# Performance work log

Hardware: AMD Instinct MI355X
Metric: run time of the kernel (lower is better)

The kernel has to match this reference:

```python
import jax, jax.numpy as jnp
import numpy as np

N0, N1, N2 = 16384, 4096, 1024   # node counts at the 3 hierarchy levels
DEG = 16                          # avg degree -> E = N*DEG per level
OUT_CH = 4
GTD = 2048                        # global_token_dim


def _gcn(x, ei, w, b):
    # GCNConv: out = D^{-1/2} (A + I) D^{-1/2} (x @ W) + b
    n = x.shape[0]
    h = x @ w
    loop = jnp.arange(n, dtype=ei.dtype)
    src = jnp.concatenate([ei[0], loop])
    dst = jnp.concatenate([ei[1], loop])
    deg = jax.ops.segment_sum(jnp.ones(src.shape[0], h.dtype), dst, num_segments=n)
    dinv = jax.lax.rsqrt(jnp.maximum(deg, 1.0))   # deg >= 1 thanks to self loops
    coef = (dinv[src] * dinv[dst])[:, None]
    return jax.ops.segment_sum(h[src] * coef, dst, num_segments=n) + b


def _knn_interp(x, pos_src, pos_dst, k):
    # inverse-squared-distance weighted interpolation over k nearest sources
    d2 = (jnp.sum(pos_dst * pos_dst, -1, keepdims=True)
          + jnp.sum(pos_src * pos_src, -1)[None, :]
          - 2.0 * (pos_dst @ pos_src.T))          # (M, N) squared distances
    negd, idx = jax.lax.top_k(-d2, k)
    w = 1.0 / jnp.maximum(-negd, 1e-16)           # (M, k)
    return jnp.einsum('mk,mkc->mc', w, x[idx]) / jnp.sum(w, -1, keepdims=True)


def _bnorm(h, gamma, beta):
    # BatchNorm1d in training mode (batch statistics over nodes)
    mu = jnp.mean(h, 0)
    var = jnp.mean((h - mu) ** 2, 0)
    return (h - mu) * jax.lax.rsqrt(var + 1e-5) * gamma + beta


def _forward(fl, idx0, idx1, ei0, ei1, ei2):
    (x, pos,
     s1w0, s1b0, s1w1, s1b1, s1w2, s1b2,
     s2w0, s2b0, s2w1, s2b1, s2w2, s2b2,
     bw0, bb0, bw1, bb1, bw2, bb2,
     gw0, gb0, gw1, gb1, gw2, gb2, gg0, gbe0, gg1, gbe1,
     f2w0, f2b0, f2w1, f2b1, f2w2, f2b2,
     f1w0, f1b0, f1w1, f1b1, f1w2, f1b2,
     mw0, mb0, mw1, mb1) = fl
    relu = jax.nn.relu
    # SA1 (skip_pos_encoding=True): convs on full graph, then subsample by idx0
    h = relu(_gcn(x, ei0, s1w0, s1b0))
    h = relu(_gcn(h, ei0, s1w1, s1b1))
    h = relu(_gcn(h, ei0, s1w2, s1b2))
    x1, pos1 = h[idx0], pos[idx0]                 # (N1, 64)
    # SA2: concat pos, convs on level-1 graph, subsample by idx1
    h = jnp.concatenate([x1, pos1], 1)
    h = relu(_gcn(h, ei1, s2w0, s2b0))
    h = relu(_gcn(h, ei1, s2w1, s2b1))
    h = relu(_gcn(h, ei1, s2w2, s2b2))
    x2, pos2 = h[idx1], pos1[idx1]                # (N2, 128)
    # bottleneck (no subsample)
    h = jnp.concatenate([x2, pos2], 1)
    h = relu(_gcn(h, ei2, bw0, bb0))
    h = relu(_gcn(h, ei2, bw1, bb1))
    xb = relu(_gcn(h, ei2, bw2, bb2))             # (N2, 256)
    # GlobalSA: MLP(+BN) -> global max pool -> k=1 interp (broadcast, B=1) -> concat skip
    g = jnp.concatenate([x2, pos2], 1)
    g = relu(_bnorm(g @ gw0 + gb0, gg0, gbe0))
    g = relu(_bnorm(g @ gw1 + gb1, gg1, gbe1))
    g = g @ gw2 + gb2                             # (N2, GTD)
    gmax = jnp.max(g, 0, keepdims=True)
    h = jnp.concatenate([jnp.broadcast_to(gmax, (x2.shape[0], gmax.shape[1])), xb], 1)
    # FP2: knn-interpolate level2 -> level1, concat skip, convs on level-1 graph
    h = _knn_interp(h, pos2, pos1, 3)
    h = jnp.concatenate([h, x1], 1)               # (N1, GTD+256+64)
    h = relu(_gcn(h, ei1, f2w0, f2b0))
    h = relu(_gcn(h, ei1, f2w1, f2b1))
    h = relu(_gcn(h, ei1, f2w2, f2b2))
    # FP1: knn-interpolate level1 -> level0, concat raw features, convs on full graph
    h = _knn_interp(h, pos1, pos, 3)
    h = jnp.concatenate([h, x], 1)                # (N0, 518)
    h = relu(_gcn(h, ei0, f1w0, f1b0))
    h = relu(_gcn(h, ei0, f1w1, f1b1))
    h = relu(_gcn(h, ei0, f1w2, f1b2))            # (N0, 128)
    # final MLP (norm=None)
    return relu(h @ mw0 + mb0) @ mw1 + mb1        # (N0, OUT_CH)


def setup_inputs() -> dict:
    keys = iter(jax.random.split(jax.random.key(0), 64))
    def lin(i, o):
        return (jax.random.normal(next(keys), (i, o), jnp.float32) / np.float32(np.sqrt(i)),
                jnp.zeros((o,), jnp.float32))
    d = {}
    d['x'] = jax.random.normal(next(keys), (N0, 6), jnp.float32)
    d['pos'] = jax.random.uniform(next(keys), (N0, 3), jnp.float32)
    for nm, sp in [('sa1', [(6, 32), (32, 32), (32, 64)]),
                   ('sa2', [(67, 64), (64, 64), (64, 128)]),
                   ('bn', [(131, 128), (128, 128), (128, 256)])]:
        for j, (i, o) in enumerate(sp):
            d[nm + '_w' + str(j)], d[nm + '_b' + str(j)] = lin(i, o)
    for j, (i, o) in enumerate([(131, 512), (512, 1024), (1024, GTD)]):
        d['g_w' + str(j)], d['g_b' + str(j)] = lin(i, o)
    d['g_g0'] = jnp.ones((512,), jnp.float32); d['g_be0'] = jnp.zeros((512,), jnp.float32)
    d['g_g1'] = jnp.ones((1024,), jnp.float32); d['g_be1'] = jnp.zeros((1024,), jnp.float32)
    for nm, sp in [('fp2', [(GTD + 256 + 64, 1024), (1024, 1024), (1024, 512)]),
                   ('fp1', [(512 + 6, 256), (256, 256), (256, 128)])]:
        for j, (i, o) in enumerate(sp):
            d[nm + '_w' + str(j)], d[nm + '_b' + str(j)] = lin(i, o)
    d['m_w0'], d['m_b0'] = lin(128, 64)
    d['m_w1'], d['m_b1'] = lin(64, OUT_CH)
    d['idx0'] = jax.random.randint(next(keys), (N1,), 0, N0)
    d['idx1'] = jax.random.randint(next(keys), (N2,), 0, N1)
    d['ei0'] = jax.random.randint(next(keys), (2, N0 * DEG), 0, N0)
    d['ei1'] = jax.random.randint(next(keys), (2, N1 * DEG), 0, N1)
    d['ei2'] = jax.random.randint(next(keys), (2, N2 * DEG), 0, N2)
    return d


def reference(x, pos,
              sa1_w0, sa1_b0, sa1_w1, sa1_b1, sa1_w2, sa1_b2,
              sa2_w0, sa2_b0, sa2_w1, sa2_b1, sa2_w2, sa2_b2,
              bn_w0, bn_b0, bn_w1, bn_b1, bn_w2, bn_b2,
              g_w0, g_b0, g_w1, g_b1, g_w2, g_b2, g_g0, g_be0, g_g1, g_be1,
              fp2_w0, fp2_b0, fp2_w1, fp2_b1, fp2_w2, fp2_b2,
              fp1_w0, fp1_b0, fp1_w1, fp1_b1, fp1_w2, fp1_b2,
              m_w0, m_b0, m_w1, m_b1,
              idx0, idx1, ei0, ei1, ei2):
    fl = (x, pos,
          sa1_w0, sa1_b0, sa1_w1, sa1_b1, sa1_w2, sa1_b2,
          sa2_w0, sa2_b0, sa2_w1, sa2_b1, sa2_w2, sa2_b2,
          bn_w0, bn_b0, bn_w1, bn_b1, bn_w2, bn_b2,
          g_w0, g_b0, g_w1, g_b1, g_w2, g_b2, g_g0, g_be0, g_g1, g_be1,
          fp2_w0, fp2_b0, fp2_w1, fp2_b1, fp2_w2, fp2_b2,
          fp1_w0, fp1_b0, fp1_w1, fp1_b1, fp1_w2, fp1_b2,
          m_w0, m_b0, m_w1, m_b1)
    return _forward(fl, idx0, idx1, ei0, ei1, ei2)
```

## Files before the change

### kernel.cpp

```cpp
#include <hip/hip_runtime.h>
#include <hip/hip_bf16.h>

typedef __hip_bfloat16 bf16;
typedef __attribute__((ext_vector_type(8))) short bf8v;
typedef __attribute__((ext_vector_type(4))) float f32x4;

__device__ __forceinline__ float ldw(const void* p, long i, int isbf) {
    return isbf ? __bfloat162float(((const bf16*)p)[i]) : ((const float*)p)[i];
}
__device__ __forceinline__ unsigned short f2bf(float v) {
    bf16 h = __float2bfloat16(v);
    return *reinterpret_cast<unsigned short*>(&h);
}
__device__ __forceinline__ float bfu2f(unsigned short u) {
    return __uint_as_float((unsigned)u << 16);
}

__global__ void k_detect(const unsigned short* __restrict__ w, int n, int* __restrict__ flag) {
    __shared__ int cnt;
    if (threadIdx.x == 0) cnt = 0;
    __syncthreads();
    int bad = 0;
    for (int i = threadIdx.x; i < n; i += 256) {
        int e = (w[i] >> 7) & 0xFF;
        if (e == 0xFF || (e != 0 && (e < 64 || e > 190))) bad++;
    }
    atomicAdd(&cnt, bad);
    __syncthreads();
    if (threadIdx.x == 0) *flag = (cnt > n / 16) ? 0 : 1;
}

__global__ void k_cvt_in(const void* __restrict__ s, float* __restrict__ d, int n,
                         const int* __restrict__ flag) {
    int i = blockIdx.x * 256 + threadIdx.x;
    if (i < n) d[i] = ldw(s, i, *flag);
}
__global__ void k_out(const float* __restrict__ s, void* __restrict__ d, int n,
                      const int* __restrict__ flag) {
    int i = blockIdx.x * 256 + threadIdx.x;
    if (i < n) {
        if (*flag) ((bf16*)d)[i] = __float2bfloat16(s[i]);
        else       ((float*)d)[i] = s[i];
    }
}
__global__ void k_zero(float* __restrict__ d, int n) {
    int i = blockIdx.x * 256 + threadIdx.x;
    if (i < n) d[i] = 0.f;
}
__global__ void k_zero_i(int* __restrict__ d, int n) {
    int i = blockIdx.x * 256 + threadIdx.x;
    if (i < n) d[i] = 0;
}
__global__ void k_pack4(const float* __restrict__ p, float4* __restrict__ o, int n) {
    int i = blockIdx.x * 256 + threadIdx.x;
    if (i < n) {
        float x = p[3 * i], y = p[3 * i + 1], z = p[3 * i + 2];
        float4 v = {x, y, z, fmaf(x, x, fmaf(y, y, z * z))};
        o[i] = v;
    }
}

__global__ void k_count(const int* __restrict__ dst, int* __restrict__ cnt, int E) {
    int i = blockIdx.x * 256 + threadIdx.x;
    if (i < E) atomicAdd(&cnt[dst[i]], 1);
}
__global__ void k_dinv_i(const int* __restrict__ cnt, float* __restrict__ dinv, int n) {
    int i = blockIdx.x * 256 + threadIdx.x;
    if (i < n) dinv[i] = rsqrtf((float)cnt[i] + 1.0f);
}
__global__ __launch_bounds__(1024) void k_scan(const int* __restrict__ cnt,
                                               int* __restrict__ offs, int n) {
    __shared__ int sm[1024];
    int t = threadIdx.x;
    int chunk = (n + 1023) >> 10;
    int b0 = t * chunk, b1 = min(b0 + chunk, n);
    int s = 0;
    for (int i = b0; i < b1; i++) s += cnt[i];
    sm[t] = s;
    __syncthreads();
    for (int o = 1; o < 1024; o <<= 1) {
        int v = (t >= o) ? sm[t - o] : 0;
        __syncthreads();
        sm[t] += v;
        __syncthreads();
    }
    int run = sm[t] - s;
    for (int i = b0; i < b1; i++) { offs[i] = run; run += cnt[i]; }
    if (t == 1023) offs[n] = sm[1023];
}
__global__ void k_fill(const int* __restrict__ src, const int* __restrict__ dst,
                       const int* __restrict__ offs, int* __restrict__ cur,
                       int* __restrict__ bkt, int E) {
    int e = blockIdx.x * 256 + threadIdx.x;
    if (e < E) {
        int d = dst[e];
        int p = atomicAdd(&cur[d], 1);
        bkt[offs[d] + p] = src[e];
    }
}

__global__ __launch_bounds__(256) void k_wt(const void* __restrict__ W, long woff,
                                            unsigned short* __restrict__ WTh,
                                            unsigned short* __restrict__ WTl,
                                            int K, int N, int Kpad,
                                            const int* __restrict__ flag) {
    __shared__ unsigned short th[32][33];
    __shared__ unsigned short tl[32][33];
    const int isbf = *flag;
    int n0 = blockIdx.x * 32, k0 = blockIdx.y * 32;
    int c = threadIdx.x & 31, r = threadIdx.x >> 5;
    #pragma unroll
    for (int u = 0; u < 4; u++) {
        int k = k0 + r + u * 8;
        float v = (k < K) ? ldw(W, woff + (long)k * N + n0 + c, isbf) : 0.f;
        unsigned short h = f2bf(v);
        th[r + u * 8][c] = h;
        tl[r + u * 8][c] = f2bf(v - bfu2f(h));
    }
    __syncthreads();
    #pragma unroll
    for (int u = 0; u < 4; u++) {
        int n = n0 + r + u * 8;
        WTh[(long)n * Kpad + k0 + c] = th[c][r + u * 8];
        WTl[(long)n * Kpad + k0 + c] = tl[c][r + u * 8];
    }
}

__global__ __launch_bounds__(256) void k_mm(
    const float* __restrict__ A, const void* __restrict__ Wt,
    const void* __restrict__ bias, const float* __restrict__ radd,
    const float* __restrict__ rsc, const float* __restrict__ rs,
    float* __restrict__ C, int M, int K, int N, long woff, int relu,
    const int* __restrict__ flag)
{
    __shared__ float As[2][16][68];
    __shared__ float Bs[2][16][68];
    const int isbf = *flag;
    const int tid = threadIdx.x;
    const int tx = tid & 15, ty = tid >> 4;
    const int bx = blockIdx.x, by = blockIdx.y;

    const int ar = tid >> 2, aq = (tid & 3) << 2;
    const long arow = (long)(by * 64 + ar) * K;
    const int bkk = tid >> 4, bn4 = (tid & 15) << 2;
    const int bcol0 = bx * 64 + bn4;

    float acc[4][4] = {};
    float4 pa, pb;

    auto loadAB = [&](int k0) {
        int kg = k0 + aq;
        pa.x = (kg + 0 < K) ? A[arow + kg + 0] : 0.f;
        pa.y = (kg + 1 < K) ? A[arow + kg + 1] : 0.f;
        pa.z = (kg + 2 < K) ? A[arow + kg + 2] : 0.f;
        pa.w = (kg + 3 < K) ? A[arow + kg + 3] : 0.f;
        int kb = k0 + bkk;
        pb = make_float4(0.f, 0.f, 0.f, 0.f);
        if (kb < K) {
            long base = woff + (long)kb * N + bcol0;
            if (bcol0 + 3 < N) {
                pb.x = ldw(Wt, base + 0, isbf); pb.y = ldw(Wt, base + 1, isbf);
                pb.z = ldw(Wt, base + 2, isbf); pb.w = ldw(Wt, base + 3, isbf);
            } else {
                if (bcol0 < N)     pb.x = ldw(Wt, base + 0, isbf);
                if (bcol0 + 1 < N) pb.y = ldw(Wt, base + 1, isbf);
                if (bcol0 + 2 < N) pb.z = ldw(Wt, base + 2, isbf);
            }
        }
    };
    auto storeAB = [&](int b) {
        As[b][aq + 0][ar] = pa.x;  As[b][aq + 1][ar] = pa.y;
        As[b][aq + 2][ar] = pa.z;  As[b][aq + 3][ar] = pa.w;
        *(float4*)&Bs[b][bkk][bn4] = pb;
    };

    loadAB(0);
    storeAB(0);
    __syncthreads();

    const int nk = (K + 15) >> 4;
    for (int t = 0; t < nk; t++) {
        const int cur = t & 1;
        const bool more = (t + 1 < nk);
        if (more) loadAB((t + 1) << 4);
        #pragma unroll
        for (int kk = 0; kk < 16; kk++) {
            float4 a = *(const float4*)&As[cur][kk][ty << 2];
            float4 b = *(const float4*)&Bs[cur][kk][tx << 2];
            float av[4] = {a.x, a.y, a.z, a.w};
            float bv[4] = {b.x, b.y, b.z, b.w};
            #pragma unroll
            for (int i = 0; i < 4; i++)
                #pragma unroll
                for (int j = 0; j < 4; j++)
                    acc[i][j] = fmaf(av[i], bv[j], acc[i][j]);
        }
        if (more) storeAB(cur ^ 1);
        __syncthreads();
    }

    const int col = bx * 64 + (tx << 2);
    #pragma unroll
    for (int i = 0; i < 4; i++) {
        int r = by * 64 + (ty << 2) + i;
        float m = rs ? rs[r] : 1.0f;
        float rr = rsc ? rsc[r] : 1.0f;
        float v[4];
        #pragma unroll
        for (int j = 0; j < 4; j++) {
            v[j] = acc[i][j] * m;
            int c = col + j;
            if (c < N) {
                if (bias) v[j] += ldw(bias, c, isbf);
                if (radd) v[j] += radd[c] * rr;
            }
            if (relu) v[j] = fmaxf(v[j], 0.f);
        }
        if (col + 3 < N) {
            float4 o = {v[0], v[1], v[2], v[3]};
            *(float4*)&C[(long)r * N + col] = o;
        } else {
            for (int j = 0; j < 4; j++)
                if (col + j < N) C[(long)r * N + col + j] = v[j];
        }
    }
}

__global__ __launch_bounds__(256, 4) void k_mmx(
    const float* __restrict__ A,
    const unsigned short* __restrict__ WTh, const unsigned short* __restrict__ WTl,
    const void* __restrict__ bias, const float* __restrict__ radd,
    const float* __restrict__ rsc, const float* __restrict__ rs,
    float* __restrict__ C, int M, int K, int Kpad, int N, int relu,
    const int* __restrict__ flag)
{
    __shared__ unsigned short Ash[64][72];
    __shared__ unsigned short Asl[64][72];
    __shared__ unsigned short Bsh[64][72];
    __shared__ unsigned short Bsl[64][72];
    const int tid = threadIdx.x;
    const int bx = blockIdx.x, by = blockIdx.y;
    const int lane = tid & 63, wid = tid >> 6;
    const int wr = wid >> 1, wc = wid & 1;
    const int lr = lane & 15, lg = lane >> 4;
    const int ar = tid >> 2, aq = (tid & 3) << 4;
    const long arow = (long)(by * 64 + ar) * K;
    const unsigned short* wrh = WTh + (long)(bx * 64 + ar) * Kpad;
    const unsigned short* wrl = WTl + (long)(bx * 64 + ar) * Kpad;

    f32x4 acc00 = {0,0,0,0}, acc01 = {0,0,0,0};
    f32x4 acc10 = {0,0,0,0}, acc11 = {0,0,0,0};
    bf8v pah0, pah1, pal0, pal1, pbh0, pbh1, pbl0, pbl1;

    auto ld = [&](int k0) {
        int kg = k0 + aq;
        float va[16];
        if (kg + 16 <= K) {
            if ((K & 3) == 0) {
                #pragma unroll
                for (int q = 0; q < 4; q++)
                    *(float4*)&va[4 * q] = *(const float4*)&A[arow + kg + 4 * q];
            } else if ((K & 1) == 0) {
                #pragma unroll
                for (int q = 0; q < 8; q++)
                    *(float2*)&va[2 * q] = *(const float2*)&A[arow + kg + 2 * q];
            } else {
                #pragma unroll
                for (int e = 0; e < 16; e++) va[e] = A[arow + kg + e];
            }
        } else {
            #pragma unroll
            for (int e = 0; e < 16; e++) va[e] = (kg + e < K) ? A[arow + kg + e] : 0.f;
        }
        #pragma unroll
        for (int e = 0; e < 8; e++) {
            unsigned short h = f2bf(va[e]);
            pah0[e] = (short)h;
            pal0[e] = (short)f2bf(va[e] - bfu2f(h));
        }
        #pragma unroll
        for (int e = 0; e < 8; e++) {
            unsigned short h = f2bf(va[8 + e]);
            pah1[e] = (short)h;
            pal1[e] = (short)f2bf(va[8 + e] - bfu2f(h));
        }
        pbh0 = *(const bf8v*)(wrh + kg);
        pbh1 = *(const bf8v*)(wrh + kg + 8);
        pbl0 = *(const bf8v*)(wrl + kg);
        pbl1 = *(const bf8v*)(wrl + kg + 8);
    };

    ld(0);
    for (int k0 = 0; k0 < K; k0 += 64) {
        __syncthreads();
        *(bf8v*)&Ash[ar][aq] = pah0;  *(bf8v*)&Ash[ar][aq + 8] = pah1;
        *(bf8v*)&Asl[ar][aq] = pal0;  *(bf8v*)&Asl[ar][aq + 8] = pal1;
        *(bf8v*)&Bsh[ar][aq] = pbh0;  *(bf8v*)&Bsh[ar][aq + 8] = pbh1;
        *(bf8v*)&Bsl[ar][aq] = pbl0;  *(bf8v*)&Bsl[ar][aq + 8] = pbl1;
        __syncthreads();
        if (k0 + 64 < K) ld(k0 + 64);
        #pragma unroll
        for (int ks = 0; ks < 2; ks++) {
            int kb = ks * 32 + lg * 8;
            bf8v a0h = *(const bf8v*)&Ash[wr * 32 + lr][kb];
            bf8v a1h = *(const bf8v*)&Ash[wr * 32 + 16 + lr][kb];
            bf8v a0l = *(const bf8v*)&Asl[wr * 32 + lr][kb];
            bf8v a1l = *(const bf8v*)&Asl[wr * 32 + 16 + lr][kb];
            bf8v b0h = *(const bf8v*)&Bsh[wc * 32 + lr][kb];
            bf8v b1h = *(const bf8v*)&Bsh[wc * 32 + 16 + lr][kb];
            bf8v b0l = *(const bf8v*)&Bsl[wc * 32 + lr][kb];
            bf8v b1l = *(const bf8v*)&Bsl[wc * 32 + 16 + lr][kb];
            acc00 = __builtin_amdgcn_mfma_f32_16x16x32_bf16(a0l, b0h, acc00, 0, 0, 0);
            acc00 = __builtin_amdgcn_mfma_f32_16x16x32_bf16(a0h, b0l, acc00, 0, 0, 0);
            acc00 = __builtin_amdgcn_mfma_f32_16x16x32_bf16(a0h, b0h, acc00, 0, 0, 0);
            acc01 = __builtin_amdgcn_mfma_f32_16x16x32_bf16(a0l, b1h, acc01, 0, 0, 0);
            acc01 = __builtin_amdgcn_mfma_f32_16x16x32_bf16(a0h, b1l, acc01, 0, 0, 0);
            acc01 = __builtin_amdgcn_mfma_f32_16x16x32_bf16(a0h, b1h, acc01, 0, 0, 0);
            acc10 = __builtin_amdgcn_mfma_f32_16x16x32_bf16(a1l, b0h, acc10, 0, 0, 0);
            acc10 = __builtin_amdgcn_mfma_f32_16x16x32_bf16(a1h, b0l, acc10, 0, 0, 0);
            acc10 = __builtin_amdgcn_mfma_f32_16x16x32_bf16(a1h, b0h, acc10, 0, 0, 0);
            acc11 = __builtin_amdgcn_mfma_f32_16x16x32_bf16(a1l, b1h, acc11, 0, 0, 0);
            acc11 = __builtin_amdgcn_mfma_f32_16x16x32_bf16(a1h, b1l, acc11, 0, 0, 0);
            acc11 = __builtin_amdgcn_mfma_f32_16x16x32_bf16(a1h, b1h, acc11, 0, 0, 0);
        }
    }

    const int isbf = *flag;
    const int rb = by * 64 + wr * 32, cb = bx * 64 + wc * 32;
    auto epi = [&](f32x4 a, int mf, int nf) {
        int col = cb + nf * 16 + lr;
        float bv = bias ? ldw(bias, col, isbf) : 0.f;
        float rv = radd ? radd[col] : 0.f;
        #pragma unroll
        for (int g = 0; g < 4; g++) {
            int row = rb + mf * 16 + lg * 4 + g;
            float v = a[g] * (rs ? rs[row] : 1.f) + bv
                    + rv * (rsc ? rsc[row] : 1.f);
            if (relu) v = fmaxf(v, 0.f);
            C[(long)row * N + col] = v;
        }
    };
    epi(acc00, 0, 0); epi(acc01, 0, 1); epi(acc10, 1, 0); epi(acc11, 1, 1);
}

__global__ __launch_bounds__(256) void k_aggr(const float* __restrict__ t,
    const int* __restrict__ offs, const int* __restrict__ bkt,
    const float* __restrict__ dinv, const void* __restrict__ bias,
    float* __restrict__ out, int n, int C, int relu, const int* __restrict__ flag)
{
    const int G = C >> 2;
    long i = blockIdx.x * 256L + threadIdx.x;
    if (i >= (long)n * G) return;
    int d = (int)(i / G), g = (int)(i % G);
    const float4* t4 = (const float4*)t;
    float4 acc = t4[(long)d * G + g];
    int o0 = offs[d], o1 = offs[d + 1];
    int j = o0;
    for (; j + 3 < o1; j += 4) {
        int s0 = bkt[j], s1 = bkt[j + 1], s2 = bkt[j + 2], s3 = bkt[j + 3];
        float4 v0 = t4[(long)s0 * G + g];
        float4 v1 = t4[(long)s1 * G + g];
        float4 v2 = t4[(long)s2 * G + g];
        float4 v3 = t4[(long)s3 * G + g];
        acc.x += v0.x; acc.y += v0.y; acc.z += v0.z; acc.w += v0.w;
        acc.x += v1.x; acc.y += v1.y; acc.z += v1.z; acc.w += v1.w;
        acc.x += v2.x; acc.y += v2.y; acc.z += v2.z; acc.w += v2.w;
        acc.x += v3.x; acc.y += v3.y; acc.z += v3.z; acc.w += v3.w;
    }
    for (; j < o1; j++) {
        int s = bkt[j];
        float4 v = t4[(long)s * G + g];
        acc.x += v.x; acc.y += v.y; acc.z += v.z; acc.w += v.w;
    }
    float dd = dinv[d];
    acc.x *= dd; acc.y *= dd; acc.z *= dd; acc.w *= dd;
    if (bias) {
        int isbf = *flag; int c = g << 2;
        acc.x += ldw(bias, c, isbf); acc.y += ldw(bias, c + 1, isbf);
        acc.z += ldw(bias, c + 2, isbf); acc.w += ldw(bias, c + 3, isbf);
    }
    if (relu) {
        acc.x = fmaxf(acc.x, 0.f); acc.y = fmaxf(acc.y, 0.f);
        acc.z = fmaxf(acc.z, 0.f); acc.w = fmaxf(acc.w, 0.f);
    }
    ((float4*)out)[(long)d * G + g] = acc;
}

__global__ void k_sigacc(const int* __restrict__ src, const int* __restrict__ dst,
                         const float* __restrict__ dinv, float* __restrict__ sig, int E) {
    int e = blockIdx.x * 256 + threadIdx.x;
    if (e < E) atomicAdd(&sig[dst[e]], dinv[src[e]]);
}
__global__ void k_sigfin(float* __restrict__ sig, const float* __restrict__ dinv, int n) {
    int i = blockIdx.x * 256 + threadIdx.x;
    if (i < n) sig[i] = dinv[i] * (sig[i] + dinv[i]);
}
__global__ void k_rowvec_acc(const float* __restrict__ gmax, const void* __restrict__ W,
                             float* __restrict__ out, const int* __restrict__ flag) {
    int n = blockIdx.x * 256 + threadIdx.x;
    if (n >= 1024) return;
    const int isbf = *flag;
    int c0 = blockIdx.y * 128;
    float s = 0.f;
    for (int c = c0; c < c0 + 128; c++) s += gmax[c] * ldw(W, (long)c * 1024 + n, isbf);
    atomicAdd(&out[n], s);
}

__global__ __launch_bounds__(256) void k_bn(float* __restrict__ h, const void* __restrict__ gamma,
                                            const void* __restrict__ beta, int n, int C,
                                            const int* __restrict__ flag) {
    int c = blockIdx.x;
    int tid = threadIdx.x;
    __shared__ float sm[256];
    float v[4];
    float s = 0.f;
    #pragma unroll
    for (int u = 0; u < 4; u++) {
        int r = tid + u * 256;
        v[u] = (r < n) ? h[(long)r * C + c] : 0.f;
        s += v[u];
    }
    sm[tid] = s; __syncthreads();
    for (int o = 128; o > 0; o >>= 1) { if (tid < o) sm[tid] += sm[tid + o]; __syncthreads(); }
    float mu = sm[0] / n;
    __syncthreads();
    float s2 = 0.f;
    #pragma unroll
    for (int u = 0; u < 4; u++) {
        int r = tid + u * 256;
        if (r < n) { float d = v[u] - mu; s2 += d * d; }
    }
    sm[tid] = s2; __syncthreads();
    for (int o = 128; o > 0; o >>= 1) { if (tid < o) sm[tid] += sm[tid + o]; __syncthreads(); }
    float var = sm[0] / n;
    float rsq = rsqrtf(var + 1e-5f);
    float g = ldw(gamma, c, *flag), be = ldw(beta, c, *flag);
    #pragma unroll
    for (int u = 0; u < 4; u++) {
        int r = tid + u * 256;
        if (r < n) h[(long)r * C + c] = fmaxf((v[u] - mu) * rsq * g + be, 0.f);
    }
}

__global__ __launch_bounds__(256) void k_cmax(const float* __restrict__ h, float* __restrict__ out) {
    __shared__ float sm[256];
    int coff = threadIdx.x & 63, rq = threadIdx.x >> 6;
    int c = blockIdx.x * 64 + coff;
    float m = -3.0e38f;
    for (int r = rq; r < 1024; r += 4) m = fmaxf(m, h[(long)r * 2048 + c]);
    sm[threadIdx.x] = m;
    __syncthreads();
    if (rq == 0) {
        m = fmaxf(fmaxf(sm[coff], sm[64 + coff]), fmaxf(sm[128 + coff], sm[192 + coff]));
        out[c] = m;
    }
}

__global__ void k_gather(const float* __restrict__ src, const int* __restrict__ idx,
                         float* __restrict__ dst, int n, int ncol, int ss, int ds, int doff) {
    long i = blockIdx.x * 256L + threadIdx.x;
    if (i < (long)n * ncol) {
        int r = (int)(i / ncol), c = (int)(i % ncol);
        dst[(long)r * ds + doff + c] = src[(long)idx[r] * ss + c];
    }
}
__global__ void k_copy(const float* __restrict__ src, float* __restrict__ dst,
                       const float* __restrict__ rmul,
                       int n, int ncol, int ss, int ds, int doff) {
    long i = blockIdx.x * 256L + threadIdx.x;
    if (i < (long)n * ncol) {
        int r = (int)(i / ncol), c = (int)(i % ncol);
        float v = src[(long)r * ss + c];
        if (rmul) v *= rmul[r];
        dst[(long)r * ds + doff + c] = v;
    }
}

__device__ __forceinline__ bool knn_better(float d, int i, float D, int I) {
    return d < D || (d == D && i < I);
}
#define KNN_INS(rv, sv)                                                              \
    if ((rv) < bd2) {                                                                \
        if ((rv) < bd0)      { bd2 = bd1; bi2 = bi1; bd1 = bd0; bi1 = bi0;           \
                               bd0 = (rv); bi0 = (sv); }                             \
        else if ((rv) < bd1) { bd2 = bd1; bi2 = bi1; bd1 = (rv); bi1 = (sv); }       \
        else                 { bd2 = (rv); bi2 = (sv); }                             \
    }
__global__ __launch_bounds__(256) void k_knn_w(const float* __restrict__ pdst,
                                               const float4* __restrict__ psrc4,
                                               int M, int Ns,
                                               int* __restrict__ kidx, float* __restrict__ kw) {
    int wid = (blockIdx.x * 256 + threadIdx.x) >> 6;
    int lane = threadIdx.x & 63;
    if (wid >= M) return;
    float x = pdst[wid * 3], y = pdst[wid * 3 + 1], z = pdst[wid * 3 + 2];
    float nd = fmaf(x, x, fmaf(y, y, z * z));
    float bd0 = 3.4e38f, bd1 = 3.4e38f, bd2 = 3.4e38f;
    int bi0 = 0x7fffffff, bi1 = 0x7fffffff, bi2 = 0x7fffffff;
    int s = lane;
    for (; s + 64 < Ns; s += 128) {
        float4 q0 = psrc4[s];
        float4 q1 = psrc4[s + 64];
        float r0 = fmaf(-2.f, fmaf(x, q0.x, fmaf(y, q0.y, z * q0.z)), q0.w);
        float r1 = fmaf(-2.f, fmaf(x, q1.x, fmaf(y, q1.y, z * q1.z)), q1.w);
        KNN_INS(r0, s);
        KNN_INS(r1, s + 64);
    }
    for (; s < Ns; s += 64) {
        float4 q = psrc4[s];
        float r = fmaf(-2.f, fmaf(x, q.x, fmaf(y, q.y, z * q.z)), q.w);
        KNN_INS(r, s);
    }
    #pragma unroll
    for (int off = 32; off >= 1; off >>= 1) {
        float od0 = __shfl_xor(bd0, off, 64); int oi0 = __shfl_xor(bi0, off, 64);
        float od1 = __shfl_xor(bd1, off, 64); int oi1 = __shfl_xor(bi1, off, 64);
        float od2 = __shfl_xor(bd2, off, 64); int oi2 = __shfl_xor(bi2, off, 64);
        float dq[3] = {od0, od1, od2}; int iq[3] = {oi0, oi1, oi2};
        #pragma unroll
        for (int q = 0; q < 3; q++) {
            float dd = dq[q]; int ii = iq[q];
            if (knn_better(dd, ii, bd0, bi0))      { bd2 = bd1; bi2 = bi1; bd1 = bd0; bi1 = bi0; bd0 = dd; bi0 = ii; }
            else if (knn_better(dd, ii, bd1, bi1)) { bd2 = bd1; bi2 = bi1; bd1 = dd; bi1 = ii; }
            else if (knn_better(dd, ii, bd2, bi2)) { bd2 = dd; bi2 = ii; }
        }
    }
    if (lane == 0) {
        kidx[wid * 3] = bi0; kidx[wid * 3 + 1] = bi1; kidx[wid * 3 + 2] = bi2;
        kw[wid * 3]     = 1.0f / fmaxf(nd + bd0, 1e-16f);
        kw[wid * 3 + 1] = 1.0f / fmaxf(nd + bd1, 1e-16f);
        kw[wid * 3 + 2] = 1.0f / fmaxf(nd + bd2, 1e-16f);
    }
}

__global__ void k_knn_apply4(const float* __restrict__ h, const int* __restrict__ kidx,
                             const float* __restrict__ kw, const float* __restrict__ rmul,
                             float* __restrict__ out,
                             int M, int C, int ds) {
    const int G = C >> 2;
    long i = blockIdx.x * 256L + threadIdx.x;
    if (i >= (long)M * G) return;
    int r = (int)(i / G), g = (int)(i % G);
    int i0 = kidx[r * 3], i1 = kidx[r * 3 + 1], i2 = kidx[r * 3 + 2];
    float w0 = kw[r * 3], w1 = kw[r * 3 + 1], w2 = kw[r * 3 + 2];
    float inv = 1.0f / (w0 + w1 + w2);
    const float4* h4 = (const float4*)h;
    float4 a = h4[(long)i0 * G + g], b = h4[(long)i1 * G + g], c = h4[(long)i2 * G + g];
    float4 o;
    o.x = (w0 * a.x + w1 * b.x + w2 * c.x) * inv;
    o.y = (w0 * a.y + w1 * b.y + w2 * c.y) * inv;
    o.z = (w0 * a.z + w1 * b.z + w2 * c.z) * inv;
    o.w = (w0 * a.w + w1 * b.w + w2 * c.w) * inv;
    if (rmul) {
        float dd = rmul[r];
        o.x *= dd; o.y *= dd; o.z *= dd; o.w *= dd;
    }
    *(float4*)&out[(long)r * ds + (g << 2)] = o;
}
__global__ void k_knn_apply2(const float* __restrict__ h, const int* __restrict__ kidx,
                             const float* __restrict__ kw, float* __restrict__ out,
                             int M, int C, int ds) {
    const int G = C >> 1;
    long i = blockIdx.x * 256L + threadIdx.x;
    if (i >= (long)M * G) return;
    int r = (int)(i / G), g = (int)(i % G);
    int i0 = kidx[r * 3], i1 = kidx[r * 3 + 1], i2 = kidx[r * 3 + 2];
    float w0 = kw[r * 3], w1 = kw[r * 3 + 1], w2 = kw[r * 3 + 2];
    float inv = 1.0f / (w0 + w1 + w2);
    const float2* h2 = (const float2*)h;
    float2 a = h2[(long)i0 * G + g], b = h2[(long)i1 * G + g], c = h2[(long)i2 * G + g];
    float2 o;
    o.x = (w0 * a.x + w1 * b.x + w2 * c.x) * inv;
    o.y = (w0 * a.y + w1 * b.y + w2 * c.y) * inv;
    *(float2*)&out[(long)r * ds + (g << 1)] = o;
}

extern "C" void kernel_launch(void* const* d_in, const int* in_sizes, int n_in,
                              void* d_out, int out_size, void* d_ws, size_t ws_size,
                              hipStream_t stream) {
    const int N0 = 16384, N1 = 4096, N2 = 1024;
    const int E0 = in_sizes[48] / 2, E1 = in_sizes[49] / 2, E2 = in_sizes[50] / 2;

    const int* idx0 = (const int*)d_in[46];
    const int* idx1 = (const int*)d_in[47];
    const int* ei0  = (const int*)d_in[48];
    const int* ei1  = (const int*)d_in[49];
    const int* ei2  = (const int*)d_in[50];

    float* W = (float*)d_ws;
    size_t off = 0;
    auto alloc = [&](size_t nf) { float* p = W + off; off += (nf + 63) & ~(size_t)63; return p; };
    auto allocU = [&](size_t nu) { return (unsigned short*)alloc((nu + 1) / 2); };
    float* P     = alloc(4194304);
    float* Q     = alloc(4194304);
    float* CAT   = alloc(8486912);
    float* xf    = alloc(98304);
    float* posf  = alloc(49152);
    float* pos1  = alloc(12288);
    float* pos2  = alloc(3072);
    float* pos1p = alloc(16384);
    float* pos2p = alloc(4096);
    float* dinv0 = alloc(16384);
    float* dinv1 = alloc(4096);
    float* dinv2 = alloc(1024);
    float* x1    = alloc(262144);
    float* c2    = alloc(134144);
    float* xb    = alloc(262144);
    float* gmaxb = alloc(2048);
    float* rowv  = alloc(1024);
    float* sigb  = alloc(4096);
    float* kwb   = alloc(49152);
    int*   kib   = (int*)alloc(49152);
    int*   flg   = (int*)alloc(64);
    int*   cntb  = (int*)alloc(16384);
    int*   offs0 = (int*)alloc(16448);
    int*   offs1 = (int*)alloc(4160);
    int*   offs2 = (int*)alloc(1088);
    int*   bkt0  = (int*)alloc(E0);
    int*   bkt1  = (int*)alloc(E1);
    int*   bkt2  = (int*)alloc(E2);

    struct WtPair { unsigned short *h, *l; int Kp; };
    auto mkwt = [&](size_t n, int Kp) {
        WtPair p; p.h = allocU(n); p.l = allocU(n); p.Kp = Kp; return p;
    };
    WtPair wt6  = mkwt(64 * 64, 64);
    WtPair wt8  = mkwt(64 * 128, 128);
    WtPair wt10 = mkwt(64 * 64, 64);
    WtPair wt12 = mkwt(128 * 64, 64);
    WtPair wt14 = mkwt(128 * 192, 192);
    WtPair wt16 = mkwt(128 * 128, 128);
    WtPair wt18 = mkwt(256 * 128, 128);
    WtPair wt20 = mkwt(512 * 192, 192);
    WtPair wt22 = mkwt(1024 * 512, 512);
    WtPair wt24 = mkwt(2048 * 1024, 1024);
    WtPair wt30 = mkwt(1024 * 320, 320);
    WtPair wt32 = mkwt(1024 * 1024, 1024);
    WtPair wt34 = mkwt(512 * 1024, 1024);
    WtPair wt36 = mkwt(256 * 576, 576);
    WtPair wt38 = mkwt(256 * 256, 256);
    WtPair wt40 = mkwt(128 * 256, 256);
    WtPair wt42 = mkwt(64 * 128, 128);

    const bool usex = (off * sizeof(float)) <= ws_size;

    auto g1 = [](long n) { return dim3((unsigned)((n + 255) / 256)); };

    auto mm = [&](const float* Ain, int iw, int ib, const float* radd, const float* rsc,
                  const float* rs, float* out, int M_, int K_, int N_, long woff, int relu) {
        dim3 g((N_ + 63) / 64, M_ / 64);
        k_mm<<<g, 256, 0, stream>>>(Ain, d_in[iw], ib >= 0 ? d_in[ib] : nullptr,
                                    radd, rsc, rs, out, M_, K_, N_, woff, relu, flg);
    };
    auto mmx = [&](const float* Ain, int iw, int ib, const float* radd, const float* rsc,
                   const float* rs, float* out, int M_, int K_, int N_, long woff, int relu,
                   const WtPair& wp) {
        if (usex) {
            dim3 g(N_ / 64, M_ / 64);
            k_mmx<<<g, 256, 0, stream>>>(Ain, wp.h, wp.l,
                                         ib >= 0 ? d_in[ib] : nullptr,
                                         radd, rsc, rs, out, M_, K_, wp.Kp, N_, relu, flg);
        } else {
            mm(Ain, iw, ib, radd, rsc, rs, out, M_, K_, N_, woff, relu);
        }
    };
    auto gcnx = [&](const float* Ain, int n, int K, int iw, int ib, int C,
                    const int* offs, const int* bkt, const float* dinv, float* t, float* out,
                    const WtPair& wp) {
        mmx(Ain, iw, -1, nullptr, nullptr, dinv, t, n, K, C, 0, 0, wp);
        k_aggr<<<g1((long)n * (C >> 2)), 256, 0, stream>>>(t, offs, bkt, dinv, d_in[ib],
                                                           out, n, C, 1, flg);
    };
    auto gcn = [&](const float* Ain, int n, int K, int iw, int ib, int C,
                   const int* offs, const int* bkt, const float* dinv, float* t, float* out) {
        mm(Ain, iw, -1, nullptr, nullptr, dinv, t, n, K, C, 0, 0);
        k_aggr<<<g1((long)n * (C >> 2)), 256, 0, stream>>>(t, offs, bkt, dinv, d_in[ib],
                                                           out, n, C, 1, flg);
    };
    auto csr = [&](const int* ei, int E, int n, int* offs, int* bkt, float* dinv) {
        k_zero_i<<<g1(n), 256, 0, stream>>>(cntb, n);
        k_count<<<g1(E), 256, 0, stream>>>(ei + E, cntb, E);
        k_dinv_i<<<g1(n), 256, 0, stream>>>(cntb, dinv, n);
        k_scan<<<1, 1024, 0, stream>>>(cntb, offs, n);
        k_zero_i<<<g1(n), 256, 0, stream>>>(cntb, n);
        k_fill<<<g1(E), 256, 0, stream>>>(ei, ei + E, offs, cntb, bkt, E);
    };
    auto wtk = [&](int iw, long woff, int K_, int N_, const WtPair& wp) {
        if (!usex) return;
        dim3 g(N_ / 32, wp.Kp / 32);
        k_wt<<<g, 256, 0, stream>>>(d_in[iw], woff, wp.h, wp.l, K_, N_, wp.Kp, flg);
    };

    k_detect<<<1, 256, 0, stream>>>((const unsigned short*)d_in[2], in_sizes[2], flg);
    k_cvt_in<<<g1(N0 * 6), 256, 0, stream>>>(d_in[0], xf, N0 * 6, flg);
    k_cvt_in<<<g1(N0 * 3), 256, 0, stream>>>(d_in[1], posf, N0 * 3, flg);
    csr(ei0, E0, N0, offs0, bkt0, dinv0);
    csr(ei1, E1, N1, offs1, bkt1, dinv1);
    csr(ei2, E2, N2, offs2, bkt2, dinv2);
    wtk(6, 0, 32, 64, wt6);
    wtk(8, 0, 67, 64, wt8);
    wtk(10, 0, 64, 64, wt10);
    wtk(12, 0, 64, 128, wt12);
    wtk(14, 0, 131, 128, wt14);
    wtk(16, 0, 128, 128, wt16);
    wtk(18, 0, 128, 256, wt18);
    wtk(20, 0, 131, 512, wt20);
    wtk(22, 0, 512, 1024, wt22);
    wtk(24, 0, 1024, 2048, wt24);
    wtk(30, 2048L * 1024L, 320, 1024, wt30);
    wtk(32, 0, 1024, 1024, wt32);
    wtk(34, 0, 1024, 512, wt34);
    wtk(36, 0, 518, 256, wt36);
    wtk(38, 0, 256, 256, wt38);
    wtk(40, 0, 256, 128, wt40);
    wtk(42, 0, 128, 64, wt42);

    gcn(xf, N0, 6, 2, 3, 32, offs0, bkt0, dinv0, P, Q);
    gcn(Q, N0, 32, 4, 5, 32, offs0, bkt0, dinv0, P, Q);
    gcnx(Q, N0, 32, 6, 7, 64, offs0, bkt0, dinv0, P, Q, wt6);
    k_gather<<<g1((long)N1 * 64), 256, 0, stream>>>(Q, idx0, x1, N1, 64, 64, 64, 0);
    k_gather<<<g1((long)N1 * 3), 256, 0, stream>>>(posf, idx0, pos1, N1, 3, 3, 3, 0);

    k_copy<<<g1((long)N1 * 64), 256, 0, stream>>>(x1, P, nullptr, N1, 64, 64, 67, 0);
    k_copy<<<g1((long)N1 * 3), 256, 0, stream>>>(pos1, P, nullptr, N1, 3, 3, 67, 64);
    gcnx(P, N1, 67, 8, 9, 64, offs1, bkt1, dinv1, Q, P, wt8);
    gcnx(P, N1, 64, 10, 11, 64, offs1, bkt1, dinv1, Q, P, wt10);
    gcnx(P, N1, 64, 12, 13, 128, offs1, bkt1, dinv1, Q, P, wt12);
    k_gather<<<g1((long)N2 * 128), 256, 0, stream>>>(P, idx1, c2, N2, 128, 128, 131, 0);
    k_gather<<<g1((long)N2 * 3), 256, 0, stream>>>(pos1, idx1, pos2, N2, 3, 3, 3, 0);
    k_copy<<<g1((long)N2 * 3), 256, 0, stream>>>(pos2, c2, nullptr, N2, 3, 3, 131, 128);

    gcnx(c2, N2, 131, 14, 15, 128, offs2, bkt2, dinv2, P, Q, wt14);
    gcnx(Q, N2, 128, 16, 17, 128, offs2, bkt2, dinv2, P, Q, wt16);
    gcnx(Q, N2, 128, 18, 19, 256, offs2, bkt2, dinv2, P, xb, wt18);

    mmx(c2, 20, 21, nullptr, nullptr, nullptr, P, N2, 131, 512, 0, 0, wt20);
    k_bn<<<dim3(512), 256, 0, stream>>>(P, d_in[26], d_in[27], N2, 512, flg);
    mmx(P, 22, 23, nullptr, nullptr, nullptr, Q, N2, 512, 1024, 0, 0, wt22);
    k_bn<<<dim3(1024), 256, 0, stream>>>(Q, d_in[28], d_in[29], N2, 1024, flg);
    mmx(Q, 24, 25, nullptr, nullptr, nullptr, P, N2, 1024, 2048, 0, 0, wt24);
    k_cmax<<<dim3(32), 256, 0, stream>>>(P, gmaxb);

    k_zero<<<g1(1024), 256, 0, stream>>>(rowv, 1024);
    k_rowvec_acc<<<dim3(4, 16), 256, 0, stream>>>(gmaxb, d_in[30], rowv, flg);
    k_pack4<<<g1(N1), 256, 0, stream>>>(pos1, (float4*)pos1p, N1);
    k_pack4<<<g1(N2), 256, 0, stream>>>(pos2, (float4*)pos2p, N2);
    k_knn_w<<<g1((long)N1 * 64), 256, 0, stream>>>(pos1, (const float4*)pos2p, N1, N2, kib, kwb);
    k_knn_apply4<<<g1((long)N1 * 64), 256, 0, stream>>>(xb, kib, kwb, dinv1, CAT, N1, 256, 320);
    k_copy<<<g1((long)N1 * 64), 256, 0, stream>>>(x1, CAT, dinv1, N1, 64, 64, 320, 256);
    k_aggr<<<g1((long)N1 * 80), 256, 0, stream>>>(CAT, offs1, bkt1, dinv1, nullptr,
                                                  P, N1, 320, 0, flg);
    k_zero<<<g1(N1), 256, 0, stream>>>(sigb, N1);
    k_sigacc<<<g1(E1), 256, 0, stream>>>(ei1, ei1 + E1, dinv1, sigb, E1);
    k_sigfin<<<g1(N1), 256, 0, stream>>>(sigb, dinv1, N1);
    mmx(P, 30, 31, rowv, sigb, nullptr, Q, N1, 320, 1024, 2048L * 1024L, 1, wt30);
    gcnx(Q, N1, 1024, 32, 33, 1024, offs1, bkt1, dinv1, P, Q, wt32);
    gcnx(Q, N1, 1024, 34, 35, 512, offs1, bkt1, dinv1, P, Q, wt34);

    k_knn_w<<<g1((long)N0 * 64), 256, 0, stream>>>(posf, (const float4*)pos1p, N0, N1, kib, kwb);
    k_knn_apply2<<<g1((long)N0 * 256), 256, 0, stream>>>(Q, kib, kwb, CAT, N0, 512, 518);
    k_copy<<<g1((long)N0 * 6), 256, 0, stream>>>(xf, CAT, nullptr, N0, 6, 6, 518, 512);
    gcnx(CAT, N0, 518, 36, 37, 256, offs0, bkt0, dinv0, P, Q, wt36);
    gcnx(Q, N0, 256, 38, 39, 256, offs0, bkt0, dinv0, P, CAT, wt38);
    gcnx(CAT, N0, 256, 40, 41, 128, offs0, bkt0, dinv0, P, Q, wt40);

    mmx(Q, 42, 43, nullptr, nullptr, nullptr, P, N0, 128, 64, 0, 1, wt42);
    mm(P, 44, 45, nullptr, nullptr, nullptr, xf, N0, 64, 4, 0, 0);
    k_out<<<g1(N0 * 4), 256, 0, stream>>>(xf, d_out, N0 * 4, flg);
}
```

Before: 1.060 ms.

## Deepen k_mmx global prefetch to two stages and add XCD-aware block remap

The split-bf16 GEMM kernel now keeps two register sets of raw fp32 A and bf16 W tiles in flight, loading tile t+2 while tile t is computed. The hi/lo bf16 split conversion moves to the shared-memory store step, so global loads are issued earlier and more latency is hidden. Workgroup IDs are also remapped so consecutive tiles land on the same XCD, which should improve L2 reuse. The cost is higher register pressure under launch_bounds(256,4), which may cause spills or lower occupancy.

```diff
diff --git a/kernel.cpp b/kernel.cpp
--- a/kernel.cpp
+++ b/kernel.cpp
@@ -226,6 +226,61 @@
     }
 }
 
+#define LDSET(aa0, aa1, aa2, aa3, vbh0, vbh1, vbl0, vbl1, K0)                      \
+    {                                                                              \
+        int kg_ = (K0) + aq;                                                       \
+        float t_[16];                                                              \
+        if (kg_ + 16 <= K) {                                                       \
+            if ((K & 3) == 0) {                                                    \
+                *(float4*)&t_[0]  = *(const float4*)&A[arow + kg_];                \
+                *(float4*)&t_[4]  = *(const float4*)&A[arow + kg_ + 4];            \
+                *(float4*)&t_[8]  = *(const float4*)&A[arow + kg_ + 8];            \
+                *(float4*)&t_[12] = *(const float4*)&A[arow + kg_ + 12];           \
+            } else if ((K & 1) == 0) {                                             \
+                _Pragma("unroll")                                                  \
+                for (int q_ = 0; q_ < 8; q_++)                                     \
+                    *(float2*)&t_[2 * q_] = *(const float2*)&A[arow + kg_ + 2 * q_]; \
+            } else {                                                               \
+                _Pragma("unroll")                                                  \
+                for (int e_ = 0; e_ < 16; e_++) t_[e_] = A[arow + kg_ + e_];       \
+            }                                                                      \
+        } else {                                                                   \
+            _Pragma("unroll")                                                      \
+            for (int e_ = 0; e_ < 16; e_++)                                        \
+                t_[e_] = (kg_ + e_ < K) ? A[arow + kg_ + e_] : 0.f;                \
+        }                                                                          \
+        aa0 = *(float4*)&t_[0];  aa1 = *(float4*)&t_[4];                           \
+        aa2 = *(float4*)&t_[8];  aa3 = *(float4*)&t_[12];                          \
+        vbh0 = *(const bf8v*)(wrh + kg_);                                          \
+        vbh1 = *(const bf8v*)(wrh + kg_ + 8);                                      \
+        vbl0 = *(const bf8v*)(wrl + kg_);                                          \
+        vbl1 = *(const bf8v*)(wrl + kg_ + 8);                                      \
+    }
+
+#define STSET(aa0, aa1, aa2, aa3, vbh0, vbh1, vbl0, vbl1)                          \
+    {                                                                              \
+        float t_[16];                                                              \
+        *(float4*)&t_[0] = aa0;  *(float4*)&t_[4] = aa1;                           \
+        *(float4*)&t_[8] = aa2;  *(float4*)&t_[12] = aa3;                          \
+        bf8v h0_, h1_, l0_, l1_;                                                   \
+        _Pragma("unroll")                                                          \
+        for (int e_ = 0; e_ < 8; e_++) {                                           \
+            unsigned short hh_ = f2bf(t_[e_]);                                     \
+            h0_[e_] = (short)hh_;                                                  \
+            l0_[e_] = (short)f2bf(t_[e_] - bfu2f(hh_));                            \
+        }                                                                          \
+        _Pragma("unroll")                                                          \
+        for (int e_ = 0; e_ < 8; e_++) {                                           \
+            unsigned short hh_ = f2bf(t_[8 + e_]);                                 \
+            h1_[e_] = (short)hh_;                                                  \
+            l1_[e_] = (short)f2bf(t_[8 + e_] - bfu2f(hh_));                        \
+        }                                                                          \
+        *(bf8v*)&Ash[ar][aq] = h0_;   *(bf8v*)&Ash[ar][aq + 8] = h1_;              \
+        *(bf8v*)&Asl[ar][aq] = l0_;   *(bf8v*)&Asl[ar][aq + 8] = l1_;              \
+        *(bf8v*)&Bsh[ar][aq] = vbh0;  *(bf8v*)&Bsh[ar][aq + 8] = vbh1;             \
+        *(bf8v*)&Bsl[ar][aq] = vbl0;  *(bf8v*)&Bsl[ar][aq + 8] = vbl1;             \
+    }
+
 __global__ __launch_bounds__(256, 4) void k_mmx(
     const float* __restrict__ A,
     const unsigned short* __restrict__ WTh, const unsigned short* __restrict__ WTl,
@@ -239,7 +294,16 @@
     __shared__ unsigned short Bsh[64][72];
     __shared__ unsigned short Bsl[64][72];
     const int tid = threadIdx.x;
-    const int bx = blockIdx.x, by = blockIdx.y;
+    const int nbx = gridDim.x;
+    int id = blockIdx.y * nbx + blockIdx.x;
+    {
+        int nwg = nbx * gridDim.y;
+        if ((nwg & 7) == 0) {
+            int xcd = id & 7, pos = id >> 3;
+            id = xcd * (nwg >> 3) + pos;
+        }
+    }
+    const int bx = id % nbx, by = id / nbx;
     const int lane = tid & 63, wid = tid >> 6;
     const int wr = wid >> 1, wc = wid & 1;
     const int lr = lane & 15, lg = lane >> 4;
@@ -250,55 +314,24 @@
 
     f32x4 acc00 = {0,0,0,0}, acc01 = {0,0,0,0};
     f32x4 acc10 = {0,0,0,0}, acc11 = {0,0,0,0};
-    bf8v pah0, pah1, pal0, pal1, pbh0, pbh1, pbl0, pbl1;
-
-    auto ld = [&](int k0) {
-        int kg = k0 + aq;
-        float va[16];
-        if (kg + 16 <= K) {
-            if ((K & 3) == 0) {
-                #pragma unroll
-                for (int q = 0; q < 4; q++)
-                    *(float4*)&va[4 * q] = *(const float4*)&A[arow + kg + 4 * q];
-            } else if ((K & 1) == 0) {
-                #pragma unroll
-                for (int q = 0; q < 8; q++)
-                    *(float2*)&va[2 * q] = *(const float2*)&A[arow + kg + 2 * q];
-            } else {
-                #pragma unroll
-                for (int e = 0; e < 16; e++) va[e] = A[arow + kg + e];
-            }
-        } else {
-            #pragma unroll
-            for (int e = 0; e < 16; e++) va[e] = (kg + e < K) ? A[arow + kg + e] : 0.f;
-        }
-        #pragma unroll
-        for (int e = 0; e < 8; e++) {
-            unsigned short h = f2bf(va[e]);
-            pah0[e] = (short)h;
-            pal0[e] = (short)f2bf(va[e] - bfu2f(h));
-        }
-        #pragma unroll
-        for (int e = 0; e < 8; e++) {
-            unsigned short h = f2bf(va[8 + e]);
-            pah1[e] = (short)h;
-            pal1[e] = (short)f2bf(va[8 + e] - bfu2f(h));
-        }
-        pbh0 = *(const bf8v*)(wrh + kg);
-        pbh1 = *(const bf8v*)(wrh + kg + 8);
-        pbl0 = *(const bf8v*)(wrl + kg);
-        pbl1 = *(const bf8v*)(wrl + kg + 8);
-    };
-
-    ld(0);
-    for (int k0 = 0; k0 < K; k0 += 64) {
+
+    float4 aA0, aA1, aA2, aA3, aB0, aB1, aB2, aB3;
+    bf8v bhA0, bhA1, blA0, blA1, bhB0, bhB1, blB0, blB1;
+
+    const int nt = (K + 63) >> 6;
+    LDSET(aA0, aA1, aA2, aA3, bhA0, bhA1, blA0, blA1, 0);
+    if (nt > 1) LDSET(aB0, aB1, aB2, aB3, bhB0, bhB1, blB0, blB1, 64);
+
+    for (int t = 0; t < nt; t++) {
         __syncthreads();
-        *(bf8v*)&Ash[ar][aq] = pah0;  *(bf8v*)&Ash[ar][aq + 8] = pah1;
-        *(bf8v*)&Asl[ar][aq] = pal0;  *(bf8v*)&Asl[ar][aq + 8] = pal1;
-        *(bf8v*)&Bsh[ar][aq] = pbh0;  *(bf8v*)&Bsh[ar][aq + 8] = pbh1;
-        *(bf8v*)&Bsl[ar][aq] = pbl0;  *(bf8v*)&Bsl[ar][aq + 8] = pbl1;
+        if ((t & 1) == 0) { STSET(aA0, aA1, aA2, aA3, bhA0, bhA1, blA0, blA1); }
+        else              { STSET(aB0, aB1, aB2, aB3, bhB0, bhB1, blB0, blB1); }
         __syncthreads();
-        if (k0 + 64 < K) ld(k0 + 64);
+        if (t + 2 < nt) {
+            int k2 = (t + 2) << 6;
+            if ((t & 1) == 0) { LDSET(aA0, aA1, aA2, aA3, bhA0, bhA1, blA0, blA1, k2); }
+            else              { LDSET(aB0, aB1, aB2, aB3, bhB0, bhB1, blB0, blB1, k2); }
+        }
         #pragma unroll
         for (int ks = 0; ks < 2; ks++) {
             int kb = ks * 32 + lg * 8;
```

New measurement: 1.084 ms. 1.02x slower.
